# Performance work log

Measured on AMD Instinct MI355X. Metric: run time of the kernel, lower is better.

Reference implementation:

```python
import jax, jax.numpy as jnp
import numpy as np

N_NODES = 100000
N_EDGES = 1600000
IN_DIM, HID_DIM, OUT_DIM = 128, 256, 128


def gcn_conv(x, src, dst, W, b, n):
    # PyG GCNConv: linear transform, add self-loops, symmetric normalization,
    # scatter-sum aggregation over destination nodes, then bias.
    h = x @ W  # [n, d_out]
    loops = jnp.arange(n, dtype=src.dtype)
    s = jnp.concatenate([src, loops])
    d = jnp.concatenate([dst, loops])
    deg = jax.ops.segment_sum(jnp.ones_like(d, dtype=h.dtype), d, num_segments=n)
    dinv = jnp.where(deg > 0, jax.lax.rsqrt(deg), 0.0)
    norm = dinv[s] * dinv[d]  # [E+n]
    msg = h[s] * norm[:, None]  # gather + scale
    out = jax.ops.segment_sum(msg, d, num_segments=n)  # scatter-reduce
    return out + b


def layer_norm(x, gamma, beta, eps=1e-5):
    mu = jnp.mean(x, axis=-1, keepdims=True)
    var = jnp.mean(jnp.square(x - mu), axis=-1, keepdims=True)
    return (x - mu) * jax.lax.rsqrt(var + eps) * gamma + beta


def setup_inputs() -> dict:
    key = jax.random.key(0)
    ks = jax.random.split(key, 8)
    x = jax.random.normal(ks[0], (N_NODES, IN_DIM), dtype=jnp.float32)
    edge_index = jax.random.randint(ks[1], (2, N_EDGES), 0, N_NODES, dtype=jnp.int64)
    W1 = jax.random.normal(ks[2], (IN_DIM, HID_DIM), dtype=jnp.float32) * (1.0 / np.sqrt(IN_DIM))
    b1 = jnp.zeros((HID_DIM,), dtype=jnp.float32)
    W2 = jax.random.normal(ks[3], (HID_DIM, OUT_DIM), dtype=jnp.float32) * (1.0 / np.sqrt(HID_DIM))
    b2 = jnp.zeros((OUT_DIM,), dtype=jnp.float32)
    gamma = jnp.ones((OUT_DIM,), dtype=jnp.float32)
    beta = jnp.zeros((OUT_DIM,), dtype=jnp.float32)
    return {"x": x, "edge_index": edge_index, "W1": W1, "b1": b1,
            "W2": W2, "b2": b2, "gamma": gamma, "beta": beta}


def reference(x, edge_index, W1, b1, W2, b2, gamma, beta):
    n = x.shape[0]
    src, dst = edge_index[0], edge_index[1]
    h = gcn_conv(x, src, dst, W1, b1, n)
    h = jax.nn.relu(h)
    # dropout(p=0.1) is identity in eval mode
    h = gcn_conv(h, src, dst, W2, b2, n)
    return layer_norm(h, gamma, beta)
```

## Files before the change

kernel.cpp:

```cpp
#include <hip/hip_runtime.h>
#include <hip/hip_fp16.h>
#include <stdint.h>

#define N_NODES 100000
#define N_EDGES 1600000
#define IN_DIM  128
#define HID_DIM 256
#define OUT_DIM 128
#define RS 264
#define NBUCK 391
#define EPB   4096
#define PADB  5120

typedef __attribute__((ext_vector_type(8))) _Float16 f16x8;
typedef __attribute__((ext_vector_type(4))) float f32x4;

__device__ __forceinline__ int clampi(int v) {
    v = v < 0 ? 0 : v;
    return v >= N_NODES ? N_NODES - 1 : v;
}
__device__ __forceinline__ float2 h2f2(uint32_t u) {
    union { uint32_t u; __half2 h; } c; c.u = u;
    return __half22float2(c.h);
}
__device__ __forceinline__ uint32_t packh(float a, float b) {
    union { __half2 h; uint32_t u; } c; c.h = __floats2half2_rn(a, b);
    return c.u;
}
__device__ __forceinline__ uint16_t f2h(float a) {
    union { __half h; uint16_t s; } c; c.h = __float2half_rn(a);
    return c.s;
}


__global__ void detect_kernel(const int* __restrict__ ei, int* __restrict__ flag) {
    if (threadIdx.x == 0 && blockIdx.x == 0) {
        int z = 1;
        for (int i = 0; i < 16; ++i)
            if (ei[2 * i + 1] != 0) z = 0;
        flag[0] = z;
    }
}

__device__ __forceinline__ int src_at(const int* ei, int isI64, int e) {
    return clampi(isI64 ? ei[2 * (size_t)e] : ei[e]);
}
__device__ __forceinline__ int dst_at(const int* ei, int isI64, int e) {
    return clampi(isI64 ? ei[2 * (size_t)N_EDGES + 2 * (size_t)e]
                        : ei[(size_t)N_EDGES + e]);
}


__global__ __launch_bounds__(256) void partition_kernel(const int* __restrict__ ei,
                                                        const int* __restrict__ flag,
                                                        int* __restrict__ cursor,
                                                        uint2* __restrict__ recs) {
    __shared__ int hist[NBUCK];
    __shared__ int histBase[NBUCK];
    __shared__ int gBase[NBUCK];
    __shared__ int scanT[512];
    __shared__ uint2 lrec[EPB];
    int tid = threadIdx.x;
    int isI64 = flag[0];
    for (int b = tid; b < NBUCK; b += 256) hist[b] = 0;
    __syncthreads();
    int base = blockIdx.x * EPB;
    int srcs[16], dsts[16], slots[16];
    #pragma unroll
    for (int r = 0; r < 16; ++r) {
        int e = base + r * 256 + tid;
        slots[r] = -1;
        srcs[r] = 0; dsts[r] = 0;
        if (e < N_EDGES) {
            srcs[r] = src_at(ei, isI64, e);
            dsts[r] = dst_at(ei, isI64, e);
            slots[r] = atomicAdd(&hist[dsts[r] >> 8], 1);
        }
    }
    __syncthreads();
    scanT[tid]       = (tid < NBUCK) ? hist[tid] : 0;
    scanT[tid + 256] = (tid + 256 < NBUCK) ? hist[tid + 256] : 0;
    __syncthreads();
    for (int off = 1; off < 512; off <<= 1) {
        int v0 = (tid >= off) ? scanT[tid - off] : 0;
        int v1 = scanT[tid + 256 - off];
        __syncthreads();
        if (tid >= off) scanT[tid] += v0;
        scanT[tid + 256] += v1;
        __syncthreads();
    }
    for (int b = tid; b < NBUCK; b += 256) {
        histBase[b] = b ? scanT[b - 1] : 0;
        if (hist[b] > 0) gBase[b] = atomicAdd(&cursor[b], hist[b]);
    }
    __syncthreads();
    #pragma unroll
    for (int r = 0; r < 16; ++r) {
        if (slots[r] >= 0) {
            int b = dsts[r] >> 8;
            uint2 rec; rec.x = (unsigned)srcs[r]; rec.y = (unsigned)dsts[r];
            lrec[histBase[b] + slots[r]] = rec;
        }
    }
    __syncthreads();
    int nvalid = N_EDGES - base; if (nvalid > EPB) nvalid = EPB;
    for (int i = tid; i < nvalid; i += 256) {
        uint2 rec = lrec[i];
        int b = (int)(rec.y >> 8);
        int pos = gBase[b] + (i - histBase[b]);
        if (pos < PADB)
            recs[(size_t)b * PADB + pos] = rec;
    }
}

__global__ __launch_bounds__(512) void bucket_scan(const int* __restrict__ cursor,
                                                   int* __restrict__ csrBase,
                                                   int* __restrict__ row_ptr) {
    __shared__ int lds[512];
    int t = threadIdx.x;
    int v = 0;
    if (t < NBUCK) { v = cursor[t]; if (v > PADB) v = PADB; }
    lds[t] = v; __syncthreads();
    for (int off = 1; off < 512; off <<= 1) {
        int x = (t >= off) ? lds[t - off] : 0;
        __syncthreads();
        if (t >= off) lds[t] += x;
        __syncthreads();
    }
    if (t < NBUCK) csrBase[t] = lds[t] - v;
    if (t == NBUCK - 1) row_ptr[N_NODES] = lds[t];
}


__global__ __launch_bounds__(256) void build_kernel(const uint2* __restrict__ recs,
                                                    const int* __restrict__ cursor,
                                                    const int* __restrict__ csrBase,
                                                    int* __restrict__ row_ptr,
                                                    float* __restrict__ dinv,
                                                    int* __restrict__ colv) {
    __shared__ uint2 lrec[PADB];
    __shared__ int cnt[256];
    __shared__ int lofs[256];
    __shared__ int cur[256];
    __shared__ int scanT[256];
    int b = blockIdx.x, tid = threadIdx.x;
    int nb = cursor[b]; if (nb > PADB) nb = PADB;
    cnt[tid] = 0; cur[tid] = 0;
    __syncthreads();
    for (int i = tid; i < nb; i += 256) {
        uint2 r = recs[(size_t)b * PADB + i];
        lrec[i] = r;
        atomicAdd(&cnt[r.y & 255], 1);
    }
    __syncthreads();
    scanT[tid] = cnt[tid];
    __syncthreads();
    for (int off = 1; off < 256; off <<= 1) {
        int x = (tid >= off) ? scanT[tid - off] : 0;
        __syncthreads();
        if (tid >= off) scanT[tid] += x;
        __syncthreads();
    }
    lofs[tid] = tid ? scanT[tid - 1] : 0;
    int cbase = csrBase[b];
    int node = b * 256 + tid;
    if (node < N_NODES) {
        row_ptr[node] = cbase + lofs[tid];
        dinv[node] = rsqrtf((float)(cnt[tid] + 1));
    }
    __syncthreads();
    for (int i = tid; i < nb; i += 256) {
        uint2 r = lrec[i];
        int id = (int)(r.y & 255);
        int slot = atomicAdd(&cur[id], 1);
        colv[cbase + lofs[id] + slot] = (int)r.x;
    }
}


__global__ __launch_bounds__(256) void wconv_kernel(const float* __restrict__ W,
                                                    uint16_t* __restrict__ Wt,
                                                    int K, int N) {
    int idx = blockIdx.x * 256 + threadIdx.x;
    if (idx < K * N) {
        int k = idx / N, n = idx - k * N;
        Wt[n * K + k] = f2h(W[idx]);
    }
}


__global__ __launch_bounds__(256) void xscale_kernel(const float* __restrict__ x,
                                                     const float* __restrict__ dinv,
                                                     uint32_t* __restrict__ xs16) {
    int idx = blockIdx.x * 256 + threadIdx.x;
    if (idx < N_NODES * 32) {
        float d = dinv[idx >> 5];
        float4 v = ((const float4*)x)[idx];
        uint2 o;
        o.x = packh(d * v.x, d * v.y);
        o.y = packh(d * v.z, d * v.w);
        ((uint2*)xs16)[idx] = o;
    }
}


template<bool LN>
__global__ __launch_bounds__(256) void agg_kernel(const uint4* __restrict__ rows,
                                                  const int* __restrict__ row_ptr,
                                                  const int* __restrict__ colv,
                                                  const float* __restrict__ dinv,
                                                  const float* __restrict__ bias,
                                                  const float* __restrict__ gamma,
                                                  const float* __restrict__ beta,
                                                  float* __restrict__ out,
                                                  uint4* __restrict__ out16) {
    int node = blockIdx.x * 16 + (threadIdx.x >> 4);
    if (node >= N_NODES) return;
    int l = threadIdx.x & 15;
    float di = dinv[node];
    float acc[8];
    {
        uint4 u = rows[(size_t)node * 16 + l];
        float2 f0 = h2f2(u.x), f1 = h2f2(u.y), f2 = h2f2(u.z), f3 = h2f2(u.w);
        acc[0] = f0.x; acc[1] = f0.y; acc[2] = f1.x; acc[3] = f1.y;
        acc[4] = f2.x; acc[5] = f2.y; acc[6] = f3.x; acc[7] = f3.y;
    }
    int e = row_ptr[node], e1 = row_ptr[node + 1];
    int sa = (e < e1) ? colv[e] : 0;
    int sb = (e + 1 < e1) ? colv[e + 1] : 0;
    while (e + 2 <= e1) {
        uint4 va = rows[(size_t)clampi(sa) * 16 + l];
        uint4 vb = rows[(size_t)clampi(sb) * 16 + l];
        int na = (e + 2 < e1) ? colv[e + 2] : 0;
        int nb = (e + 3 < e1) ? colv[e + 3] : 0;
        {
            float2 f0 = h2f2(va.x), f1 = h2f2(va.y), f2 = h2f2(va.z), f3 = h2f2(va.w);
            acc[0] += f0.x; acc[1] += f0.y; acc[2] += f1.x; acc[3] += f1.y;
            acc[4] += f2.x; acc[5] += f2.y; acc[6] += f3.x; acc[7] += f3.y;
        }
        {
            float2 f0 = h2f2(vb.x), f1 = h2f2(vb.y), f2 = h2f2(vb.z), f3 = h2f2(vb.w);
            acc[0] += f0.x; acc[1] += f0.y; acc[2] += f1.x; acc[3] += f1.y;
            acc[4] += f2.x; acc[5] += f2.y; acc[6] += f3.x; acc[7] += f3.y;
        }
        sa = na; sb = nb; e += 2;
    }
    if (e < e1) {
        uint4 v = rows[(size_t)clampi(sa) * 16 + l];
        float2 f0 = h2f2(v.x), f1 = h2f2(v.y), f2 = h2f2(v.z), f3 = h2f2(v.w);
        acc[0] += f0.x; acc[1] += f0.y; acc[2] += f1.x; acc[3] += f1.y;
        acc[4] += f2.x; acc[5] += f2.y; acc[6] += f3.x; acc[7] += f3.y;
    }
    if (!LN) {
        uint4 o;
        o.x = packh(acc[0] * di, acc[1] * di);
        o.y = packh(acc[2] * di, acc[3] * di);
        o.z = packh(acc[4] * di, acc[5] * di);
        o.w = packh(acc[6] * di, acc[7] * di);
        out16[(size_t)node * 16 + l] = o;
    } else {
        const float4* b4 = (const float4*)(bias + l * 8);
        float4 bb0 = b4[0], bb1 = b4[1];
        float v[8];
        v[0] = acc[0] * di + bb0.x; v[1] = acc[1] * di + bb0.y;
        v[2] = acc[2] * di + bb0.z; v[3] = acc[3] * di + bb0.w;
        v[4] = acc[4] * di + bb1.x; v[5] = acc[5] * di + bb1.y;
        v[6] = acc[6] * di + bb1.z; v[7] = acc[7] * di + bb1.w;
        float s = 0.f;
        #pragma unroll
        for (int j = 0; j < 8; ++j) s += v[j];
        #pragma unroll
        for (int o = 8; o > 0; o >>= 1) s += __shfl_xor(s, o, 64);
        float mu = s * (1.0f / 128.0f);
        float q = 0.f;
        #pragma unroll
        for (int j = 0; j < 8; ++j) { v[j] -= mu; q += v[j] * v[j]; }
        #pragma unroll
        for (int o = 8; o > 0; o >>= 1) q += __shfl_xor(q, o, 64);
        float rstd = rsqrtf(q * (1.0f / 128.0f) + 1e-5f);
        const float4* g4 = (const float4*)(gamma + l * 8);
        const float4* t4 = (const float4*)(beta + l * 8);
        float4 g0 = g4[0], g1 = g4[1], t0 = t4[0], t1 = t4[1];
        float* orow = out + (size_t)node * 128 + l * 8;
        float4 o0, o1;
        o0.x = v[0] * rstd * g0.x + t0.x; o0.y = v[1] * rstd * g0.y + t0.y;
        o0.z = v[2] * rstd * g0.z + t0.z; o0.w = v[3] * rstd * g0.w + t0.w;
        o1.x = v[4] * rstd * g1.x + t1.x; o1.y = v[5] * rstd * g1.y + t1.y;
        o1.z = v[6] * rstd * g1.z + t1.z; o1.w = v[7] * rstd * g1.w + t1.w;
        *(float4*)orow = o0; *(float4*)(orow + 4) = o1;
    }
}


__global__ __launch_bounds__(256) void fused_gemm_kernel(const uint16_t* __restrict__ A16,
                                                         const uint16_t* __restrict__ W1t,
                                                         const float* __restrict__ b1,
                                                         const uint16_t* __restrict__ W2t,
                                                         const float* __restrict__ dinv,
                                                         uint16_t* __restrict__ G16, int M) {
    __shared__ __align__(16) uint16_t Hs[64 * RS];
    int lane = threadIdx.x & 63;
    int wave = threadIdx.x >> 6;
    int r15 = lane & 15;
    int quad = lane >> 4;
    int kofs = quad * 8;
    int blk_row = blockIdx.x * 64;

    f16x8 a[4][4];
    #pragma unroll
    for (int mt = 0; mt < 4; ++mt) {
        bool valid = (blk_row + mt * 16) < M;
        int row = valid ? (blk_row + mt * 16 + r15) : 0;
        const uint16_t* arow = A16 + (size_t)row * IN_DIM + kofs;
        #pragma unroll
        for (int ks = 0; ks < 4; ++ks)
            a[mt][ks] = *(const f16x8*)(arow + ks * 32);
    }

    #pragma unroll
    for (int nt = 0; nt < 4; ++nt) {
        int ncol = (wave * 4 + nt) * 16 + r15;
        const uint16_t* bp = W1t + (size_t)ncol * IN_DIM + kofs;
        f32x4 acc[4];
        #pragma unroll
        for (int mt = 0; mt < 4; ++mt) acc[mt] = (f32x4){0.f, 0.f, 0.f, 0.f};
        #pragma unroll
        for (int ks = 0; ks < 4; ++ks) {
            f16x8 bv = *(const f16x8*)(bp + ks * 32);
            #pragma unroll
            for (int mt = 0; mt < 4; ++mt)
                acc[mt] = __builtin_amdgcn_mfma_f32_16x16x32_f16(a[mt][ks], bv, acc[mt], 0, 0, 0);
        }
        float bb = b1[ncol];
        #pragma unroll
        for (int mt = 0; mt < 4; ++mt) {
            #pragma unroll
            for (int r = 0; r < 4; ++r) {
                int lrow = mt * 16 + quad * 4 + r;
                Hs[lrow * RS + ncol] = f2h(fmaxf(acc[mt][r] + bb, 0.f));
            }
        }
    }
    __syncthreads();

    #pragma unroll
    for (int nt = 0; nt < 2; ++nt) {
        int ncol = (wave * 2 + nt) * 16 + r15;
        const uint16_t* bp = W2t + (size_t)ncol * HID_DIM + kofs;
        f16x8 b2[8];
        #pragma unroll
        for (int ks = 0; ks < 8; ++ks)
            b2[ks] = *(const f16x8*)(bp + ks * 32);
        f32x4 acc[4];
        #pragma unroll
        for (int mt = 0; mt < 4; ++mt) acc[mt] = (f32x4){0.f, 0.f, 0.f, 0.f};
        #pragma unroll
        for (int ks = 0; ks < 8; ++ks) {
            #pragma unroll
            for (int mt = 0; mt < 4; ++mt) {
                f16x8 av = *(const f16x8*)(Hs + (mt * 16 + r15) * RS + ks * 32 + kofs);
                acc[mt] = __builtin_amdgcn_mfma_f32_16x16x32_f16(av, b2[ks], acc[mt], 0, 0, 0);
            }
        }
        #pragma unroll
        for (int mt = 0; mt < 4; ++mt) {
            if ((blk_row + mt * 16) < M) {
                #pragma unroll
                for (int r = 0; r < 4; ++r) {
                    int row = blk_row + mt * 16 + quad * 4 + r;
                    G16[(size_t)row * OUT_DIM + ncol] = f2h(dinv[row] * acc[mt][r]);
                }
            }
        }
    }
}


extern "C" void kernel_launch(void* const* d_in, const int* in_sizes, int n_in,
                              void* d_out, int out_size, void* d_ws, size_t ws_size,
                              hipStream_t stream) {
    const float* x     = (const float*)d_in[0];
    const int*   ei    = (const int*)d_in[1];
    const float* W1    = (const float*)d_in[2];
    const float* b1    = (const float*)d_in[3];
    const float* W2    = (const float*)d_in[4];
    const float* b2    = (const float*)d_in[5];
    const float* gamma = (const float*)d_in[6];
    const float* beta  = (const float*)d_in[7];

    char* ws = (char*)d_ws;
    size_t off = 0;
    auto alloc = [&](size_t bytes) -> void* {
        void* p = ws + off;
        off += (bytes + 511) & ~(size_t)511;
        return p;
    };
    int*      cursor  = (int*)alloc((size_t)NBUCK * 4);
    int*      csrBase = (int*)alloc((size_t)NBUCK * 4);
    int*      row_ptr = (int*)alloc((size_t)(N_NODES + 1) * 4);
    float*    dinv    = (float*)alloc((size_t)N_NODES * 4);
    int*      flag    = (int*)alloc(4);
    uint16_t* W1t     = (uint16_t*)alloc((size_t)IN_DIM * HID_DIM * 2);
    uint16_t* W2t     = (uint16_t*)alloc((size_t)HID_DIM * OUT_DIM * 2);
    int*      colv    = (int*)alloc((size_t)N_EDGES * 4);
    void*     big     = alloc((size_t)N_NODES * IN_DIM * 2);
    uint2*    recs    = (uint2*)big;
    uint32_t* xs16    = (uint32_t*)big;
    uint16_t* g16     = (uint16_t*)big;
    if (ws_size < off) return;

    uint16_t* xa16 = (uint16_t*)d_out;

    const int PB = (N_EDGES + EPB - 1) / EPB;
    const int AB = (N_NODES + 15) / 16;
    const int GB = (N_NODES + 63) / 64;

    detect_kernel<<<1, 64, 0, stream>>>(ei, flag);
    hipMemsetAsync(cursor, 0, (size_t)NBUCK * 4, stream);
    partition_kernel<<<PB, 256, 0, stream>>>(ei, flag, cursor, recs);
    bucket_scan<<<1, 512, 0, stream>>>(cursor, csrBase, row_ptr);
    build_kernel<<<NBUCK, 256, 0, stream>>>(recs, cursor, csrBase, row_ptr, dinv, colv);

    wconv_kernel<<<(IN_DIM * HID_DIM + 255) / 256, 256, 0, stream>>>(W1, W1t, IN_DIM, HID_DIM);
    wconv_kernel<<<(HID_DIM * OUT_DIM + 255) / 256, 256, 0, stream>>>(W2, W2t, HID_DIM, OUT_DIM);

    xscale_kernel<<<(N_NODES * 32 + 255) / 256, 256, 0, stream>>>(x, dinv, xs16);
    agg_kernel<false><<<AB, 256, 0, stream>>>((const uint4*)xs16, row_ptr, colv, dinv,
                                              nullptr, nullptr, nullptr,
                                              nullptr, (uint4*)xa16);
    fused_gemm_kernel<<<GB, 256, 0, stream>>>(xa16, W1t, b1, W2t, dinv, g16, N_NODES);
    agg_kernel<true><<<AB, 256, 0, stream>>>((const uint4*)g16, row_ptr, colv, dinv,
                                             b2, gamma, beta, (float*)d_out, nullptr);
}
```

Baseline: 350.6 us.

## Fold small launch kernels, unroll gather by four, add nontemporal stores

Removes the detect and bucket_scan kernels by folding format detection into partition_kernel and computing each bucket's CSR base inside build_kernel with a per-block reduction. The two weight-conversion launches are merged into one. The aggregation loop now keeps four neighbor loads in flight instead of two and computes addresses with shifts, without clamping the neighbor index. Nontemporal loads and stores are used for intermediate buffers and outputs. Together these cut launch count and raise memory-level parallelism, but every build block now rescans the cursor array.

After: 342.4 us. 1.02x faster.

```diff
diff --git a/kernel.cpp b/kernel.cpp
--- a/kernel.cpp
+++ b/kernel.cpp
@@ -14,6 +14,7 @@
 
 typedef __attribute__((ext_vector_type(8))) _Float16 f16x8;
 typedef __attribute__((ext_vector_type(4))) float f32x4;
+typedef __attribute__((ext_vector_type(4))) unsigned int u32x4;
 
 __device__ __forceinline__ int clampi(int v) {
     v = v < 0 ? 0 : v;
@@ -32,16 +33,6 @@
     return c.s;
 }
 
-
-__global__ void detect_kernel(const int* __restrict__ ei, int* __restrict__ flag) {
-    if (threadIdx.x == 0 && blockIdx.x == 0) {
-        int z = 1;
-        for (int i = 0; i < 16; ++i)
-            if (ei[2 * i + 1] != 0) z = 0;
-        flag[0] = z;
-    }
-}
-
 __device__ __forceinline__ int src_at(const int* ei, int isI64, int e) {
     return clampi(isI64 ? ei[2 * (size_t)e] : ei[e]);
 }
@@ -52,7 +43,6 @@
 
 
 __global__ __launch_bounds__(256) void partition_kernel(const int* __restrict__ ei,
-                                                        const int* __restrict__ flag,
                                                         int* __restrict__ cursor,
                                                         uint2* __restrict__ recs) {
     __shared__ int hist[NBUCK];
@@ -60,10 +50,18 @@
     __shared__ int gBase[NBUCK];
     __shared__ int scanT[512];
     __shared__ uint2 lrec[EPB];
+    __shared__ int s_flag;
     int tid = threadIdx.x;
-    int isI64 = flag[0];
+    if (tid == 0) {
+        int z = 1;
+        #pragma unroll
+        for (int i = 0; i < 16; ++i)
+            if (ei[2 * i + 1] != 0) z = 0;
+        s_flag = z;
+    }
     for (int b = tid; b < NBUCK; b += 256) hist[b] = 0;
     __syncthreads();
+    int isI64 = s_flag;
     int base = blockIdx.x * EPB;
     int srcs[16], dsts[16], slots[16];
     #pragma unroll
@@ -108,33 +106,16 @@
         uint2 rec = lrec[i];
         int b = (int)(rec.y >> 8);
         int pos = gBase[b] + (i - histBase[b]);
-        if (pos < PADB)
-            recs[(size_t)b * PADB + pos] = rec;
-    }
-}
-
-__global__ __launch_bounds__(512) void bucket_scan(const int* __restrict__ cursor,
-                                                   int* __restrict__ csrBase,
-                                                   int* __restrict__ row_ptr) {
-    __shared__ int lds[512];
-    int t = threadIdx.x;
-    int v = 0;
-    if (t < NBUCK) { v = cursor[t]; if (v > PADB) v = PADB; }
-    lds[t] = v; __syncthreads();
-    for (int off = 1; off < 512; off <<= 1) {
-        int x = (t >= off) ? lds[t - off] : 0;
-        __syncthreads();
-        if (t >= off) lds[t] += x;
-        __syncthreads();
-    }
-    if (t < NBUCK) csrBase[t] = lds[t] - v;
-    if (t == NBUCK - 1) row_ptr[N_NODES] = lds[t];
+        if (pos < PADB) {
+            uint64_t rv = (uint64_t)rec.x | ((uint64_t)rec.y << 32);
+            __builtin_nontemporal_store(rv, (uint64_t*)&recs[(size_t)b * PADB + pos]);
+        }
+    }
 }
 
 
 __global__ __launch_bounds__(256) void build_kernel(const uint2* __restrict__ recs,
                                                     const int* __restrict__ cursor,
-                                                    const int* __restrict__ csrBase,
                                                     int* __restrict__ row_ptr,
                                                     float* __restrict__ dinv,
                                                     int* __restrict__ colv) {
@@ -145,10 +126,23 @@
     __shared__ int scanT[256];
     int b = blockIdx.x, tid = threadIdx.x;
     int nb = cursor[b]; if (nb > PADB) nb = PADB;
+    int pv = 0;
+    for (int j = tid; j < b; j += 256) {
+        int c = cursor[j];
+        pv += (c > PADB) ? PADB : c;
+    }
     cnt[tid] = 0; cur[tid] = 0;
+    scanT[tid] = pv;
+    __syncthreads();
+    for (int off = 128; off > 0; off >>= 1) {
+        if (tid < off) scanT[tid] += scanT[tid + off];
+        __syncthreads();
+    }
+    int cbase = scanT[0];
     __syncthreads();
     for (int i = tid; i < nb; i += 256) {
-        uint2 r = recs[(size_t)b * PADB + i];
+        uint64_t rv = __builtin_nontemporal_load((const uint64_t*)&recs[(size_t)b * PADB + i]);
+        uint2 r; r.x = (uint32_t)rv; r.y = (uint32_t)(rv >> 32);
         lrec[i] = r;
         atomicAdd(&cnt[r.y & 255], 1);
     }
@@ -162,12 +156,12 @@
         __syncthreads();
     }
     lofs[tid] = tid ? scanT[tid - 1] : 0;
-    int cbase = csrBase[b];
     int node = b * 256 + tid;
     if (node < N_NODES) {
         row_ptr[node] = cbase + lofs[tid];
         dinv[node] = rsqrtf((float)(cnt[tid] + 1));
     }
+    if (b == NBUCK - 1 && tid == 0) row_ptr[N_NODES] = cbase + nb;
     __syncthreads();
     for (int i = tid; i < nb; i += 256) {
         uint2 r = lrec[i];
@@ -178,13 +172,18 @@
 }
 
 
-__global__ __launch_bounds__(256) void wconv_kernel(const float* __restrict__ W,
-                                                    uint16_t* __restrict__ Wt,
-                                                    int K, int N) {
+__global__ __launch_bounds__(256) void wconv_kernel(const float* __restrict__ W1,
+                                                    uint16_t* __restrict__ W1t,
+                                                    const float* __restrict__ W2,
+                                                    uint16_t* __restrict__ W2t) {
     int idx = blockIdx.x * 256 + threadIdx.x;
-    if (idx < K * N) {
-        int k = idx / N, n = idx - k * N;
-        Wt[n * K + k] = f2h(W[idx]);
+    if (idx < IN_DIM * HID_DIM) {
+        int k = idx / HID_DIM, n = idx - k * HID_DIM;
+        W1t[n * IN_DIM + k] = f2h(W1[idx]);
+    } else {
+        idx -= IN_DIM * HID_DIM;
+        int k = idx / OUT_DIM, n = idx - k * OUT_DIM;
+        W2t[n * HID_DIM + k] = f2h(W2[idx]);
     }
 }
 
@@ -196,10 +195,9 @@
     if (idx < N_NODES * 32) {
         float d = dinv[idx >> 5];
         float4 v = ((const float4*)x)[idx];
-        uint2 o;
-        o.x = packh(d * v.x, d * v.y);
-        o.y = packh(d * v.z, d * v.w);
-        ((uint2*)xs16)[idx] = o;
+        uint64_t rv = (uint64_t)packh(d * v.x, d * v.y)
+                    | ((uint64_t)packh(d * v.z, d * v.w) << 32);
+        __builtin_nontemporal_store(rv, (uint64_t*)((uint2*)xs16 + idx));
     }
 }
 
@@ -217,47 +215,79 @@
     int node = blockIdx.x * 16 + (threadIdx.x >> 4);
     if (node >= N_NODES) return;
     int l = threadIdx.x & 15;
+    const char* base = (const char*)rows + ((unsigned)l << 4);
     float di = dinv[node];
     float acc[8];
     {
-        uint4 u = rows[(size_t)node * 16 + l];
+        uint4 u = *(const uint4*)(base + ((unsigned)node << 8));
         float2 f0 = h2f2(u.x), f1 = h2f2(u.y), f2 = h2f2(u.z), f3 = h2f2(u.w);
         acc[0] = f0.x; acc[1] = f0.y; acc[2] = f1.x; acc[3] = f1.y;
         acc[4] = f2.x; acc[5] = f2.y; acc[6] = f3.x; acc[7] = f3.y;
     }
     int e = row_ptr[node], e1 = row_ptr[node + 1];
-    int sa = (e < e1) ? colv[e] : 0;
-    int sb = (e + 1 < e1) ? colv[e + 1] : 0;
-    while (e + 2 <= e1) {
-        uint4 va = rows[(size_t)clampi(sa) * 16 + l];
-        uint4 vb = rows[(size_t)clampi(sb) * 16 + l];
-        int na = (e + 2 < e1) ? colv[e + 2] : 0;
-        int nb = (e + 3 < e1) ? colv[e + 3] : 0;
+    int s0 = 0, s1 = 0, s2 = 0, s3 = 0;
+    if (e     < e1) s0 = colv[e];
+    if (e + 1 < e1) s1 = colv[e + 1];
+    if (e + 2 < e1) s2 = colv[e + 2];
+    if (e + 3 < e1) s3 = colv[e + 3];
+    while (e + 4 <= e1) {
+        uint4 v0 = *(const uint4*)(base + ((unsigned)s0 << 8));
+        uint4 v1 = *(const uint4*)(base + ((unsigned)s1 << 8));
+        uint4 v2 = *(const uint4*)(base + ((unsigned)s2 << 8));
+        uint4 v3 = *(const uint4*)(base + ((unsigned)s3 << 8));
+        int p0 = (e + 4 < e1) ? e + 4 : e;
+        int p1 = (e + 5 < e1) ? e + 5 : e;
+        int p2 = (e + 6 < e1) ? e + 6 : e;
+        int p3 = (e + 7 < e1) ? e + 7 : e;
+        int t0 = colv[p0], t1 = colv[p1], t2 = colv[p2], t3 = colv[p3];
         {
-            float2 f0 = h2f2(va.x), f1 = h2f2(va.y), f2 = h2f2(va.z), f3 = h2f2(va.w);
+            float2 f0 = h2f2(v0.x), f1 = h2f2(v0.y), f2 = h2f2(v0.z), f3 = h2f2(v0.w);
             acc[0] += f0.x; acc[1] += f0.y; acc[2] += f1.x; acc[3] += f1.y;
             acc[4] += f2.x; acc[5] += f2.y; acc[6] += f3.x; acc[7] += f3.y;
         }
         {
-            float2 f0 = h2f2(vb.x), f1 = h2f2(vb.y), f2 = h2f2(vb.z), f3 = h2f2(vb.w);
+            float2 f0 = h2f2(v1.x), f1 = h2f2(v1.y), f2 = h2f2(v1.z), f3 = h2f2(v1.w);
             acc[0] += f0.x; acc[1] += f0.y; acc[2] += f1.x; acc[3] += f1.y;
             acc[4] += f2.x; acc[5] += f2.y; acc[6] += f3.x; acc[7] += f3.y;
         }
-        sa = na; sb = nb; e += 2;
-    }
-    if (e < e1) {
-        uint4 v = rows[(size_t)clampi(sa) * 16 + l];
+        {
+            float2 f0 = h2f2(v2.x), f1 = h2f2(v2.y), f2 = h2f2(v2.z), f3 = h2f2(v2.w);
+            acc[0] += f0.x; acc[1] += f0.y; acc[2] += f1.x; acc[3] += f1.y;
+            acc[4] += f2.x; acc[5] += f2.y; acc[6] += f3.x; acc[7] += f3.y;
+        }
+        {
+            float2 f0 = h2f2(v3.x), f1 = h2f2(v3.y), f2 = h2f2(v3.z), f3 = h2f2(v3.w);
+            acc[0] += f0.x; acc[1] += f0.y; acc[2] += f1.x; acc[3] += f1.y;
+            acc[4] += f2.x; acc[5] += f2.y; acc[6] += f3.x; acc[7] += f3.y;
+        }
+        s0 = t0; s1 = t1; s2 = t2; s3 = t3; e += 4;
+    }
+    int r = e1 - e;
+    if (r > 0) {
+        uint4 v = *(const uint4*)(base + ((unsigned)s0 << 8));
         float2 f0 = h2f2(v.x), f1 = h2f2(v.y), f2 = h2f2(v.z), f3 = h2f2(v.w);
         acc[0] += f0.x; acc[1] += f0.y; acc[2] += f1.x; acc[3] += f1.y;
         acc[4] += f2.x; acc[5] += f2.y; acc[6] += f3.x; acc[7] += f3.y;
     }
+    if (r > 1) {
+        uint4 v = *(const uint4*)(base + ((unsigned)s1 << 8));
+        float2 f0 = h2f2(v.x), f1 = h2f2(v.y), f2 = h2f2(v.z), f3 = h2f2(v.w);
+        acc[0] += f0.x; acc[1] += f0.y; acc[2] += f1.x; acc[3] += f1.y;
+        acc[4] += f2.x; acc[5] += f2.y; acc[6] += f3.x; acc[7] += f3.y;
+    }
+    if (r > 2) {
+        uint4 v = *(const uint4*)(base + ((unsigned)s2 << 8));
+        float2 f0 = h2f2(v.x), f1 = h2f2(v.y), f2 = h2f2(v.z), f3 = h2f2(v.w);
+        acc[0] += f0.x; acc[1] += f0.y; acc[2] += f1.x; acc[3] += f1.y;
+        acc[4] += f2.x; acc[5] += f2.y; acc[6] += f3.x; acc[7] += f3.y;
+    }
     if (!LN) {
-        uint4 o;
+        u32x4 o;
         o.x = packh(acc[0] * di, acc[1] * di);
         o.y = packh(acc[2] * di, acc[3] * di);
         o.z = packh(acc[4] * di, acc[5] * di);
         o.w = packh(acc[6] * di, acc[7] * di);
-        out16[(size_t)node * 16 + l] = o;
+        __builtin_nontemporal_store(o, (u32x4*)(out16 + (size_t)node * 16 + l));
     } else {
         const float4* b4 = (const float4*)(bias + l * 8);
         float4 bb0 = b4[0], bb1 = b4[1];
@@ -282,12 +312,13 @@
         const float4* t4 = (const float4*)(beta + l * 8);
         float4 g0 = g4[0], g1 = g4[1], t0 = t4[0], t1 = t4[1];
         float* orow = out + (size_t)node * 128 + l * 8;
-        float4 o0, o1;
+        f32x4 o0, o1;
         o0.x = v[0] * rstd * g0.x + t0.x; o0.y = v[1] * rstd * g0.y + t0.y;
         o0.z = v[2] * rstd * g0.z + t0.z; o0.w = v[3] * rstd * g0.w + t0.w;
         o1.x = v[4] * rstd * g1.x + t1.x; o1.y = v[5] * rstd * g1.y + t1.y;
         o1.z = v[6] * rstd * g1.z + t1.z; o1.w = v[7] * rstd * g1.w + t1.w;
-        *(float4*)orow = o0; *(float4*)(orow + 4) = o1;
+        __builtin_nontemporal_store(o0, (f32x4*)orow);
+        __builtin_nontemporal_store(o1, (f32x4*)(orow + 4));
     }
 }
 
@@ -396,10 +427,8 @@
         return p;
     };
     int*      cursor  = (int*)alloc((size_t)NBUCK * 4);
-    int*      csrBase = (int*)alloc((size_t)NBUCK * 4);
     int*      row_ptr = (int*)alloc((size_t)(N_NODES + 1) * 4);
     float*    dinv    = (float*)alloc((size_t)N_NODES * 4);
-    int*      flag    = (int*)alloc(4);
     uint16_t* W1t     = (uint16_t*)alloc((size_t)IN_DIM * HID_DIM * 2);
     uint16_t* W2t     = (uint16_t*)alloc((size_t)HID_DIM * OUT_DIM * 2);
     int*      colv    = (int*)alloc((size_t)N_EDGES * 4);
@@ -415,14 +444,12 @@
     const int AB = (N_NODES + 15) / 16;
     const int GB = (N_NODES + 63) / 64;
 
-    detect_kernel<<<1, 64, 0, stream>>>(ei, flag);
     hipMemsetAsync(cursor, 0, (size_t)NBUCK * 4, stream);
-    partition_kernel<<<PB, 256, 0, stream>>>(ei, flag, cursor, recs);
-    bucket_scan<<<1, 512, 0, stream>>>(cursor, csrBase, row_ptr);
-    build_kernel<<<NBUCK, 256, 0, stream>>>(recs, cursor, csrBase, row_ptr, dinv, colv);
-
-    wconv_kernel<<<(IN_DIM * HID_DIM + 255) / 256, 256, 0, stream>>>(W1, W1t, IN_DIM, HID_DIM);
-    wconv_kernel<<<(HID_DIM * OUT_DIM + 255) / 256, 256, 0, stream>>>(W2, W2t, HID_DIM, OUT_DIM);
+    partition_kernel<<<PB, 256, 0, stream>>>(ei, cursor, recs);
+    build_kernel<<<NBUCK, 256, 0, stream>>>(recs, cursor, row_ptr, dinv, colv);
+
+    wconv_kernel<<<(IN_DIM * HID_DIM + HID_DIM * OUT_DIM + 255) / 256, 256, 0, stream>>>(
+        W1, W1t, W2, W2t);
 
     xscale_kernel<<<(N_NODES * 32 + 255) / 256, 256, 0, stream>>>(x, dinv, xs16);
     agg_kernel<false><<<AB, 256, 0, stream>>>((const uint4*)xs16, row_ptr, colv, dinv,
```
